# Optimization experiments

Measured on AMD Instinct MI355X. Metric: run time of the kernel, lower is better.

Reference implementation:

```python
import jax, jax.numpy as jnp
import numpy as np

D_MODEL, D_LOW, NUM_BINS = 512, 64, 39
DIST_MIN, DIST_MAX = 2.0, 22.0
BIN_WIDTH = (DIST_MAX - DIST_MIN) / (NUM_BINS - 1)
LN_EPS = 1e-5


def setup_inputs() -> dict:
    key = jax.random.key(0)
    ks = jax.random.split(key, 10)
    B, N = 2, 768
    h_res = jax.random.normal(ks[0], (B, N, D_MODEL), dtype=jnp.float32)
    # scale coords so pairwise distances span the [2, 22] bin range
    x_true = jax.random.normal(ks[1], (B, N, 3), dtype=jnp.float32) * 5.0
    token_pad_mask = jnp.ones((B, N), dtype=jnp.float32)
    s = 1.0 / np.sqrt(D_MODEL)
    return {
        "h_res": h_res,
        "x_true": x_true,
        "token_pad_mask": token_pad_mask,
        "ln_w": jnp.ones((D_MODEL,), jnp.float32),
        "ln_b": jnp.zeros((D_MODEL,), jnp.float32),
        "wu_w": jax.random.normal(ks[2], (D_LOW, D_MODEL), jnp.float32) * s,
        "wu_b": jnp.zeros((D_LOW,), jnp.float32),
        "wv_w": jax.random.normal(ks[3], (D_LOW, D_MODEL), jnp.float32) * s,
        "wv_b": jnp.zeros((D_LOW,), jnp.float32),
        "wb_w": jax.random.normal(ks[4], (NUM_BINS, D_LOW), jnp.float32) * (1.0 / np.sqrt(D_LOW)),
        "wb_b": jnp.zeros((NUM_BINS,), jnp.float32),
    }


def _layernorm(x, w, b):
    mu = jnp.mean(x, axis=-1, keepdims=True)
    var = jnp.mean(jnp.square(x - mu), axis=-1, keepdims=True)
    return (x - mu) * jax.lax.rsqrt(var + LN_EPS) * w + b


def reference(h_res, x_true, token_pad_mask, ln_w, ln_b, wu_w, wu_b, wv_w, wv_b, wb_w, wb_b):
    B, N, _ = h_res.shape
    # pairwise distances -> target bins (trunc-to-int then clamp, as torch .long())
    diff = x_true[:, :, None, :] - x_true[:, None, :, :]          # [B,N,N,3]
    d_true = jnp.sqrt(jnp.sum(diff * diff, axis=-1))               # [B,N,N]
    target = jnp.clip(((d_true - DIST_MIN) / BIN_WIDTH).astype(jnp.int32), 0, NUM_BINS - 1)

    h = _layernorm(h_res, ln_w, ln_b)
    U = h @ wu_w.T + wu_b                                          # [B,N,d_low]
    V = h @ wv_w.T + wv_b                                          # [B,N,d_low]
    # logits[b,i,j,k] = sum_c U[b,i,c] V[b,j,c] Wb[k,c] + bb[k]
    logits = jnp.einsum("bic,bjc,kc->bijk", U, V, wb_w) + wb_b     # [B,N,N,K]
    logp = jax.nn.log_softmax(logits, axis=-1)
    ce = -jnp.take_along_axis(logp, target[..., None], axis=-1)[..., 0]  # [B,N,N]

    mask = (token_pad_mask[:, :, None] * token_pad_mask[:, None, :]) > 0  # [B,N,N] bool
    counts = jnp.sum(mask, axis=(1, 2))                            # [B]
    per_sample = jnp.sum(jnp.where(mask, ce, 0.0), axis=(1, 2)) / jnp.maximum(counts, 1)
    valid = counts > 0
    total_count = jnp.sum(valid)
    loss = jnp.sum(jnp.where(valid, per_sample, 0.0)) / jnp.maximum(total_count, 1)
    return loss
```

## Files before the change

### kernel.cpp

```cpp
#include <hip/hip_runtime.h>
#include <hip/hip_bf16.h>
#include <math.h>

#define D_MODEL 512
#define D_LOW   64
#define NBINS   39
#define LOG2E   1.4426950408889634f
#define LN2     0.6931471805599453f

typedef __attribute__((ext_vector_type(8))) short short8;
typedef __attribute__((ext_vector_type(4))) float floatx4;

__global__ __launch_bounds__(256) void lnproj_tbin_kernel(
    const float* __restrict__ h_res,
    const float* __restrict__ ln_w, const float* __restrict__ ln_b,
    const float* __restrict__ wu_w, const float* __restrict__ wu_b,
    const float* __restrict__ wv_w, const float* __restrict__ wv_b,
    const float* __restrict__ x_true, const float* __restrict__ pmask,
    float* __restrict__ U, __hip_bfloat16* __restrict__ Vbf,
    signed char* __restrict__ tbg, int N, int B, int nLN, int TB) {
  const int tid = threadIdx.x;

  if ((int)blockIdx.x >= nLN) {
    const int idx   = blockIdx.x - nLN;
    const int NN    = N * N;
    const int total = B * NN;
    const float BW  = (22.0f - 2.0f) / 38.0f;
    for (int p = idx * 256 + tid; p < total; p += TB * 256) {
      const int b = p / NN;
      const int r = p - b * NN;
      const int i = r / N;
      const int j = r - i * N;
      const int rowi = b * N + i, rowj = b * N + j;
      const float dx = x_true[rowi * 3 + 0] - x_true[rowj * 3 + 0];
      const float dy = x_true[rowi * 3 + 1] - x_true[rowj * 3 + 1];
      const float dz = x_true[rowi * 3 + 2] - x_true[rowj * 3 + 2];
      const float d  = sqrtf(dx * dx + dy * dy + dz * dz);
      int tb = (int)((d - 2.0f) / BW);
      tb = tb < 0 ? 0 : (tb > NBINS - 1 ? NBINS - 1 : tb);
      const bool ok = (pmask[rowi] * pmask[rowj]) > 0.f;
      tbg[p] = ok ? (signed char)tb : (signed char)-1;
    }
    return;
  }

  const int wave = tid >> 6, lane = tid & 63;
  const int q = lane >> 4, ln16 = lane & 15;
  const int row0 = blockIdx.x * 16;
  const float* hp = h_res + (size_t)(row0 + ln16) * D_MODEL + q * 8;

  short8 abf[16];
  float sum = 0.f, ssq = 0.f;
  #pragma unroll
  for (int kc = 0; kc < 16; ++kc) {
    const floatx4 x0 = *reinterpret_cast<const floatx4*>(hp + kc * 32);
    const floatx4 x1 = *reinterpret_cast<const floatx4*>(hp + kc * 32 + 4);
    short8 a;
    #pragma unroll
    for (int e = 0; e < 4; ++e) {
      sum += x0[e]; ssq += x0[e] * x0[e];
      const __hip_bfloat16 hb = __float2bfloat16(x0[e]);
      a[e] = *reinterpret_cast<const short*>(&hb);
    }
    #pragma unroll
    for (int e = 0; e < 4; ++e) {
      sum += x1[e]; ssq += x1[e] * x1[e];
      const __hip_bfloat16 hb = __float2bfloat16(x1[e]);
      a[4 + e] = *reinterpret_cast<const short*>(&hb);
    }
    abf[kc] = a;
  }
  sum += __shfl_xor(sum, 16); sum += __shfl_xor(sum, 32);
  ssq += __shfl_xor(ssq, 16); ssq += __shfl_xor(ssq, 32);
  const float mu  = sum * (1.0f / (float)D_MODEL);
  const float var = ssq * (1.0f / (float)D_MODEL) - mu * mu;
  const float rs  = rsqrtf(var + 1e-5f);
  float mu_r[4], rs_r[4];
  #pragma unroll
  for (int r = 0; r < 4; ++r) {
    mu_r[r] = __shfl(mu, q * 4 + r);
    rs_r[r] = __shfl(rs, q * 4 + r);
  }

  const int obase = wave * 32;
  const int out0 = obase + ln16;
  const int out1 = obase + 16 + ln16;
  const float* wr0 = (out0 < 64) ? (wu_w + out0 * D_MODEL) : (wv_w + (out0 - 64) * D_MODEL);
  const float* wr1 = (out1 < 64) ? (wu_w + out1 * D_MODEL) : (wv_w + (out1 - 64) * D_MODEL);
  const float sc0 = (out0 < 64) ? LOG2E : 1.0f;
  const float sc1 = (out1 < 64) ? LOG2E : 1.0f;

  floatx4 acc0 = (floatx4){0.f, 0.f, 0.f, 0.f};
  floatx4 acc1 = (floatx4){0.f, 0.f, 0.f, 0.f};
  float s1a = 0.f, s1b = 0.f;
  float s2a = 0.f, s2b = 0.f;
  #pragma unroll
  for (int kc = 0; kc < 16; ++kc) {
    const int c0 = kc * 32 + q * 8;
    const floatx4 lw0 = *reinterpret_cast<const floatx4*>(ln_w + c0);
    const floatx4 lw1 = *reinterpret_cast<const floatx4*>(ln_w + c0 + 4);
    const floatx4 lb0 = *reinterpret_cast<const floatx4*>(ln_b + c0);
    const floatx4 lb1 = *reinterpret_cast<const floatx4*>(ln_b + c0 + 4);
    const floatx4 wa0 = *reinterpret_cast<const floatx4*>(wr0 + c0);
    const floatx4 wa1 = *reinterpret_cast<const floatx4*>(wr0 + c0 + 4);
    const floatx4 wb0 = *reinterpret_cast<const floatx4*>(wr1 + c0);
    const floatx4 wb1 = *reinterpret_cast<const floatx4*>(wr1 + c0 + 4);
    short8 b0, b1;
    #pragma unroll
    for (int e = 0; e < 4; ++e) {
      const float v0 = wa0[e] * lw0[e] * sc0;
      const float v1 = wa1[e] * lw1[e] * sc0;
      const __hip_bfloat16 h0 = __float2bfloat16(v0);
      const __hip_bfloat16 h1 = __float2bfloat16(v1);
      b0[e]     = *reinterpret_cast<const short*>(&h0);
      b0[4 + e] = *reinterpret_cast<const short*>(&h1);
      s1a += __bfloat162float(h0) + __bfloat162float(h1);
      s2a += wa0[e] * lb0[e] + wa1[e] * lb1[e];
      const float u0 = wb0[e] * lw0[e] * sc1;
      const float u1 = wb1[e] * lw1[e] * sc1;
      const __hip_bfloat16 g0 = __float2bfloat16(u0);
      const __hip_bfloat16 g1 = __float2bfloat16(u1);
      b1[e]     = *reinterpret_cast<const short*>(&g0);
      b1[4 + e] = *reinterpret_cast<const short*>(&g1);
      s1b += __bfloat162float(g0) + __bfloat162float(g1);
      s2b += wb0[e] * lb0[e] + wb1[e] * lb1[e];
    }
    acc0 = __builtin_amdgcn_mfma_f32_16x16x32_bf16(abf[kc], b0, acc0, 0, 0, 0);
    acc1 = __builtin_amdgcn_mfma_f32_16x16x32_bf16(abf[kc], b1, acc1, 0, 0, 0);
  }
  s1a += __shfl_xor(s1a, 16); s1a += __shfl_xor(s1a, 32);
  s1b += __shfl_xor(s1b, 16); s1b += __shfl_xor(s1b, 32);
  s2a += __shfl_xor(s2a, 16); s2a += __shfl_xor(s2a, 32);
  s2b += __shfl_xor(s2b, 16); s2b += __shfl_xor(s2b, 32);
  const float bias0 = sc0 * (((out0 < 64) ? wu_b[out0] : wv_b[out0 - 64]) + s2a);
  const float bias1 = sc1 * (((out1 < 64) ? wu_b[out1] : wv_b[out1 - 64]) + s2b);

  #pragma unroll
  for (int nt = 0; nt < 2; ++nt) {
    const int out  = nt ? out1 : out0;
    const floatx4 a = nt ? acc1 : acc0;
    const float ws = nt ? s1b : s1a;
    const float bb = nt ? bias1 : bias0;
    #pragma unroll
    for (int r = 0; r < 4; ++r) {
      const int rowg = row0 + q * 4 + r;
      const float val = rs_r[r] * a[r] - mu_r[r] * rs_r[r] * ws + bb;
      if (out < 64) {
        U[(size_t)rowg * D_LOW + out] = val;
      } else {
        Vbf[(size_t)rowg * D_LOW + (out - 64)] = __float2bfloat16(val);
      }
    }
  }
}

__global__ __launch_bounds__(256) void wprep_kernel(
    const float* __restrict__ U, const float* __restrict__ wb_w,
    short* __restrict__ wfragbuf, int BN) {
  __shared__ float wsh[NBINS * 65];
  const int tid = threadIdx.x;
  for (int e = tid; e < NBINS * D_LOW; e += 256) {
    const int n = e >> 6, c = e & 63;
    wsh[n * 65 + c] = wb_w[e];
  }
  __syncthreads();

  const int wave = tid >> 6, lane = tid & 63;
  const int q = lane >> 4, ln16 = lane & 15;
  const int rowi = blockIdx.x * 4 + wave;
  const float* Up = U + (size_t)rowi * D_LOW;

  float u[16];
  #pragma unroll
  for (int s = 0; s < 2; ++s)
    #pragma unroll
    for (int e = 0; e < 8; ++e) u[s * 8 + e] = Up[s * 32 + q * 8 + e];

  short* outp = wfragbuf + (size_t)rowi * 6 * 64 * 8;
  #pragma unroll
  for (int t = 0; t < 3; ++t) {
    const int n = t * 16 + ln16;
    #pragma unroll
    for (int s = 0; s < 2; ++s) {
      short8 f;
      #pragma unroll
      for (int e = 0; e < 8; ++e) {
        const float w = (n < NBINS) ? wsh[n * 65 + s * 32 + q * 8 + e] : 0.f;
        const float v = u[s * 8 + e] * w;
        const __hip_bfloat16 hb = __float2bfloat16(v);
        f[e] = *reinterpret_cast<const short*>(&hb);
      }
      *reinterpret_cast<short8*>(outp + ((size_t)(t * 2 + s) * 64 + lane) * 8) = f;
    }
  }
}

__global__ __launch_bounds__(256) void pair_mfma_kernel(
    const short* __restrict__ wfragbuf,
    const __hip_bfloat16* __restrict__ Vbf,
    const float* __restrict__ wb_b,
    const signed char* __restrict__ tbg,
    float* __restrict__ part, int N) {
  __shared__ float rbuf[8];
  const int i    = blockIdx.x;
  const int b    = blockIdx.y >> 1;
  const int half = blockIdx.y & 1;
  const int tid  = threadIdx.x;
  const int wave = tid >> 6, lane = tid & 63;
  const int q = lane >> 4, ln16 = lane & 15;
  const int rowi = b * N + i;

  short8 wfrag[3][2];
  {
    const short* wfp = wfragbuf + (size_t)rowi * 6 * 64 * 8;
    #pragma unroll
    for (int t = 0; t < 3; ++t)
      #pragma unroll
      for (int s = 0; s < 2; ++s)
        wfrag[t][s] = *reinterpret_cast<const short8*>(
            wfp + ((size_t)(t * 2 + s) * 64 + lane) * 8);
  }

  floatx4 bias_init[3];
  #pragma unroll
  for (int t = 0; t < 3; ++t)
    #pragma unroll
    for (int r = 0; r < 4; ++r) {
      const int bin = t * 16 + q * 4 + r;
      bias_init[t][r] = (bin < NBINS) ? LOG2E * wb_b[bin] : -INFINITY;
    }

  const short* Vp = reinterpret_cast<const short*>(Vbf) + (size_t)b * N * D_LOW;
  const signed char* tbp = tbg + (size_t)b * N * N + (size_t)i * N;
  const int jbase = half * 384 + wave * 96;
  const int q4 = q * 4;

  float ce_sum = 0.f, cnt_sum = 0.f;

  short8 v[2][2];
  int tbv[2];
  {
    #pragma unroll
    for (int tt = 0; tt < 2; ++tt) {
      const size_t jr = jbase + tt * 16 + ln16;
      v[tt][0] = *reinterpret_cast<const short8*>(Vp + jr * D_LOW + q * 8);
      v[tt][1] = *reinterpret_cast<const short8*>(Vp + jr * D_LOW + 32 + q * 8);
      tbv[tt]  = (int)tbp[jr];
    }
  }

  for (int g = 0; g < 3; ++g) {
    short8 vn[2][2];
    int tbn[2];
    if (g < 2) {
      const int jb = jbase + (g + 1) * 32;
      #pragma unroll
      for (int tt = 0; tt < 2; ++tt) {
        const size_t jr = jb + tt * 16 + ln16;
        vn[tt][0] = *reinterpret_cast<const short8*>(Vp + jr * D_LOW + q * 8);
        vn[tt][1] = *reinterpret_cast<const short8*>(Vp + jr * D_LOW + 32 + q * 8);
        tbn[tt]   = (int)tbp[jr];
      }
    }

    floatx4 f[2][3];
    #pragma unroll
    for (int tt = 0; tt < 2; ++tt)
      #pragma unroll
      for (int t = 0; t < 3; ++t) {
        floatx4 a = bias_init[t];
        a = __builtin_amdgcn_mfma_f32_16x16x32_bf16(wfrag[t][0], v[tt][0], a, 0, 0, 0);
        a = __builtin_amdgcn_mfma_f32_16x16x32_bf16(wfrag[t][1], v[tt][1], a, 0, 0, 0);
        f[tt][t] = a;
      }

    #pragma unroll
    for (int tt = 0; tt < 2; ++tt) {
      const int tb  = tbv[tt];
      const int tbq = tb - q4;
      float s0 = 0.f, s1 = 0.f, s2 = 0.f, s3 = 0.f, lt = 0.f;
      #pragma unroll
      for (int t = 0; t < 3; ++t) {
        const floatx4 fv = f[tt][t];
        s0 += __builtin_amdgcn_exp2f(fv[0]);
        s1 += __builtin_amdgcn_exp2f(fv[1]);
        s2 += __builtin_amdgcn_exp2f(fv[2]);
        s3 += __builtin_amdgcn_exp2f(fv[3]);
        lt += (tbq == t * 16 + 0) ? fv[0] : 0.f;
        lt += (tbq == t * 16 + 1) ? fv[1] : 0.f;
        lt += (tbq == t * 16 + 2) ? fv[2] : 0.f;
        lt += (tbq == t * 16 + 3) ? fv[3] : 0.f;
      }
      float ssum = (s0 + s1) + (s2 + s3);
      ssum += __shfl_xor(ssum, 16); ssum += __shfl_xor(ssum, 32);
      const float ok = (tb >= 0) ? 1.f : 0.f;
      ce_sum  += ok * LN2 * (__builtin_amdgcn_logf(ssum) - 4.0f * lt);
      cnt_sum += ok;
    }

    if (g < 2) {
      #pragma unroll
      for (int tt = 0; tt < 2; ++tt) {
        v[tt][0] = vn[tt][0]; v[tt][1] = vn[tt][1]; tbv[tt] = tbn[tt];
      }
    }
  }

  #pragma unroll
  for (int off = 32; off; off >>= 1) {
    ce_sum  += __shfl_xor(ce_sum, off);
    cnt_sum += __shfl_xor(cnt_sum, off);
  }
  if (lane == 0) { rbuf[wave] = ce_sum; rbuf[4 + wave] = cnt_sum; }
  __syncthreads();
  if (tid == 0) {
    const size_t slot = ((size_t)(b * 2 + half) * N + i) * 2;
    part[slot + 0] = rbuf[0] + rbuf[1] + rbuf[2] + rbuf[3];
    part[slot + 1] = rbuf[4] + rbuf[5] + rbuf[6] + rbuf[7];
  }
}

__global__ __launch_bounds__(256) void finalize_kernel(
    const float* __restrict__ part, float* __restrict__ out, int N, int B) {
  __shared__ float red[8];
  const int tid = threadIdx.x, wave = tid >> 6, lane = tid & 63;
  float loss = 0.f, vcount = 0.f;
  for (int b = 0; b < B; ++b) {
    float ce = 0.f, cnt = 0.f;
    for (int e = tid; e < 2 * N; e += 256) {
      const size_t base = ((size_t)b * 2 * N + e) * 2;
      ce  += part[base + 0];
      cnt += part[base + 1];
    }
    #pragma unroll
    for (int off = 32; off; off >>= 1) {
      ce  += __shfl_xor(ce, off);
      cnt += __shfl_xor(cnt, off);
    }
    if (lane == 0) { red[wave] = ce; red[4 + wave] = cnt; }
    __syncthreads();
    if (tid == 0) {
      const float s = red[0] + red[1] + red[2] + red[3];
      const float c = red[4] + red[5] + red[6] + red[7];
      if (c > 0.f) { loss += s / fmaxf(c, 1.f); vcount += 1.f; }
    }
    __syncthreads();
  }
  if (tid == 0) out[0] = (vcount > 0.f) ? loss / vcount : 0.f;
}

extern "C" void kernel_launch(void* const* d_in, const int* in_sizes, int n_in,
                              void* d_out, int out_size, void* d_ws, size_t ws_size,
                              hipStream_t stream) {
  const float* h_res  = (const float*)d_in[0];
  const float* x_true = (const float*)d_in[1];
  const float* pmask  = (const float*)d_in[2];
  const float* ln_w   = (const float*)d_in[3];
  const float* ln_b   = (const float*)d_in[4];
  const float* wu_w   = (const float*)d_in[5];
  const float* wu_b   = (const float*)d_in[6];
  const float* wv_w   = (const float*)d_in[7];
  const float* wv_b   = (const float*)d_in[8];
  const float* wb_w   = (const float*)d_in[9];
  const float* wb_b   = (const float*)d_in[10];

  const int B  = 2;
  const int N  = in_sizes[2] / B;
  const int BN = B * N;
  const int nLN = BN / 16;
  const int TB  = 160;

  float* U = (float*)d_ws;
  __hip_bfloat16* Vbf = (__hip_bfloat16*)(U + (size_t)BN * D_LOW);
  float* part = (float*)(Vbf + (size_t)BN * D_LOW);
  signed char* tbg = (signed char*)(part + 4 * (size_t)BN);
  short* wfragbuf = (short*)(tbg + (size_t)B * N * N);

  lnproj_tbin_kernel<<<nLN + TB, 256, 0, stream>>>(
      h_res, ln_w, ln_b, wu_w, wu_b, wv_w, wv_b, x_true, pmask,
      U, Vbf, tbg, N, B, nLN, TB);
  wprep_kernel<<<BN / 4, 256, 0, stream>>>(U, wb_w, wfragbuf, BN);
  pair_mfma_kernel<<<dim3(N, 2 * B), 256, 0, stream>>>(wfragbuf, Vbf, wb_b,
                                                       tbg, part, N);
  finalize_kernel<<<1, 256, 0, stream>>>(part, (float*)d_out, N, B);
}
```

Before: 125.6 us.

## Precompute LN-folded bf16 projection weights once and split LN-projection into its own kernel

Folding ln_w and the log2e scale into bf16 weights, plus the bias and weight-sum terms, moves into a new prep kernel that runs once per output column. Before, every row-tile block redid this work. The projection becomes a separate 64-thread kernel with four blocks per row tile, which loads the prepared bf16 fragments directly. Target-bin computation is restructured to one block per row i, so the per-element divisions and repeated x_i loads go away. The cost is one extra kernel launch and a dependency between prep and projection.

Result: faster. 118.5 us (-5.6%).

```diff
diff --git a/kernel.cpp b/kernel.cpp
--- a/kernel.cpp
+++ b/kernel.cpp
@@ -11,42 +11,79 @@
 typedef __attribute__((ext_vector_type(8))) short short8;
 typedef __attribute__((ext_vector_type(4))) float floatx4;
 
-__global__ __launch_bounds__(256) void lnproj_tbin_kernel(
-    const float* __restrict__ h_res,
+__global__ __launch_bounds__(256) void prep_tbin_kernel(
     const float* __restrict__ ln_w, const float* __restrict__ ln_b,
     const float* __restrict__ wu_w, const float* __restrict__ wu_b,
     const float* __restrict__ wv_w, const float* __restrict__ wv_b,
     const float* __restrict__ x_true, const float* __restrict__ pmask,
-    float* __restrict__ U, __hip_bfloat16* __restrict__ Vbf,
-    signed char* __restrict__ tbg, int N, int B, int nLN, int TB) {
+    __hip_bfloat16* __restrict__ w2bf, float* __restrict__ w2sum,
+    float* __restrict__ b2, signed char* __restrict__ tbg, int N) {
   const int tid = threadIdx.x;
 
-  if ((int)blockIdx.x >= nLN) {
-    const int idx   = blockIdx.x - nLN;
-    const int NN    = N * N;
-    const int total = B * NN;
+  if ((int)blockIdx.x >= 128) {
+    const int p = blockIdx.x - 128;
+    const int b = (p >= N) ? 1 : 0;
+    const int i = p - b * N;
+    const int rowi = b * N + i;
+    const float xi0 = x_true[rowi * 3 + 0];
+    const float xi1 = x_true[rowi * 3 + 1];
+    const float xi2 = x_true[rowi * 3 + 2];
+    const float pmi = pmask[rowi];
     const float BW  = (22.0f - 2.0f) / 38.0f;
-    for (int p = idx * 256 + tid; p < total; p += TB * 256) {
-      const int b = p / NN;
-      const int r = p - b * NN;
-      const int i = r / N;
-      const int j = r - i * N;
-      const int rowi = b * N + i, rowj = b * N + j;
-      const float dx = x_true[rowi * 3 + 0] - x_true[rowj * 3 + 0];
-      const float dy = x_true[rowi * 3 + 1] - x_true[rowj * 3 + 1];
-      const float dz = x_true[rowi * 3 + 2] - x_true[rowj * 3 + 2];
+    signed char* tbp = tbg + (size_t)b * N * N + (size_t)i * N;
+    for (int j = tid; j < N; j += 256) {
+      const int rowj = b * N + j;
+      const float dx = xi0 - x_true[rowj * 3 + 0];
+      const float dy = xi1 - x_true[rowj * 3 + 1];
+      const float dz = xi2 - x_true[rowj * 3 + 2];
       const float d  = sqrtf(dx * dx + dy * dy + dz * dz);
       int tb = (int)((d - 2.0f) / BW);
       tb = tb < 0 ? 0 : (tb > NBINS - 1 ? NBINS - 1 : tb);
-      const bool ok = (pmask[rowi] * pmask[rowj]) > 0.f;
-      tbg[p] = ok ? (signed char)tb : (signed char)-1;
+      tbp[j] = (pmi * pmask[rowj] > 0.f) ? (signed char)tb : (signed char)-1;
     }
     return;
   }
 
+  __shared__ float red[8];
+  const int o = blockIdx.x;
+  const bool isU = (o < 64);
+  const float* wrow = isU ? (wu_w + o * D_MODEL) : (wv_w + (o - 64) * D_MODEL);
+  const float scale = isU ? LOG2E : 1.0f;
+
+  float s1 = 0.f, s2 = 0.f;
+  #pragma unroll
+  for (int cc = 0; cc < 2; ++cc) {
+    const int c = tid + cc * 256;
+    const float w  = wrow[c];
+    const float w2 = w * ln_w[c] * scale;
+    const __hip_bfloat16 hb = __float2bfloat16(w2);
+    w2bf[o * D_MODEL + c] = hb;
+    s1 += __bfloat162float(hb);
+    s2 += w * ln_b[c];
+  }
+  #pragma unroll
+  for (int off = 32; off; off >>= 1) {
+    s1 += __shfl_xor(s1, off);
+    s2 += __shfl_xor(s2, off);
+  }
   const int wave = tid >> 6, lane = tid & 63;
+  if (lane == 0) { red[wave] = s1; red[4 + wave] = s2; }
+  __syncthreads();
+  if (tid == 0) {
+    w2sum[o] = red[0] + red[1] + red[2] + red[3];
+    const float ss2 = red[4] + red[5] + red[6] + red[7];
+    b2[o] = scale * ((isU ? wu_b[o] : wv_b[o - 64]) + ss2);
+  }
+}
+
+__global__ __launch_bounds__(64) void lnproj_kernel(
+    const float* __restrict__ h_res, const __hip_bfloat16* __restrict__ w2bf,
+    const float* __restrict__ w2sum, const float* __restrict__ b2,
+    float* __restrict__ U, __hip_bfloat16* __restrict__ Vbf, int N) {
+  const int lane = threadIdx.x;
   const int q = lane >> 4, ln16 = lane & 15;
-  const int row0 = blockIdx.x * 16;
+  const int rt = blockIdx.x >> 2, og = blockIdx.x & 3;
+  const int row0 = rt * 16;
   const float* hp = h_res + (size_t)(row0 + ln16) * D_MODEL + q * 8;
 
   short8 abf[16];
@@ -82,65 +119,28 @@
     rs_r[r] = __shfl(rs, q * 4 + r);
   }
 
-  const int obase = wave * 32;
+  const int obase = og * 32;
   const int out0 = obase + ln16;
   const int out1 = obase + 16 + ln16;
-  const float* wr0 = (out0 < 64) ? (wu_w + out0 * D_MODEL) : (wv_w + (out0 - 64) * D_MODEL);
-  const float* wr1 = (out1 < 64) ? (wu_w + out1 * D_MODEL) : (wv_w + (out1 - 64) * D_MODEL);
-  const float sc0 = (out0 < 64) ? LOG2E : 1.0f;
-  const float sc1 = (out1 < 64) ? LOG2E : 1.0f;
-
+  const short* wp = reinterpret_cast<const short*>(w2bf);
   floatx4 acc0 = (floatx4){0.f, 0.f, 0.f, 0.f};
   floatx4 acc1 = (floatx4){0.f, 0.f, 0.f, 0.f};
-  float s1a = 0.f, s1b = 0.f;
-  float s2a = 0.f, s2b = 0.f;
   #pragma unroll
   for (int kc = 0; kc < 16; ++kc) {
-    const int c0 = kc * 32 + q * 8;
-    const floatx4 lw0 = *reinterpret_cast<const floatx4*>(ln_w + c0);
-    const floatx4 lw1 = *reinterpret_cast<const floatx4*>(ln_w + c0 + 4);
-    const floatx4 lb0 = *reinterpret_cast<const floatx4*>(ln_b + c0);
-    const floatx4 lb1 = *reinterpret_cast<const floatx4*>(ln_b + c0 + 4);
-    const floatx4 wa0 = *reinterpret_cast<const floatx4*>(wr0 + c0);
-    const floatx4 wa1 = *reinterpret_cast<const floatx4*>(wr0 + c0 + 4);
-    const floatx4 wb0 = *reinterpret_cast<const floatx4*>(wr1 + c0);
-    const floatx4 wb1 = *reinterpret_cast<const floatx4*>(wr1 + c0 + 4);
-    short8 b0, b1;
-    #pragma unroll
-    for (int e = 0; e < 4; ++e) {
-      const float v0 = wa0[e] * lw0[e] * sc0;
-      const float v1 = wa1[e] * lw1[e] * sc0;
-      const __hip_bfloat16 h0 = __float2bfloat16(v0);
-      const __hip_bfloat16 h1 = __float2bfloat16(v1);
-      b0[e]     = *reinterpret_cast<const short*>(&h0);
-      b0[4 + e] = *reinterpret_cast<const short*>(&h1);
-      s1a += __bfloat162float(h0) + __bfloat162float(h1);
-      s2a += wa0[e] * lb0[e] + wa1[e] * lb1[e];
-      const float u0 = wb0[e] * lw0[e] * sc1;
-      const float u1 = wb1[e] * lw1[e] * sc1;
-      const __hip_bfloat16 g0 = __float2bfloat16(u0);
-      const __hip_bfloat16 g1 = __float2bfloat16(u1);
-      b1[e]     = *reinterpret_cast<const short*>(&g0);
-      b1[4 + e] = *reinterpret_cast<const short*>(&g1);
-      s1b += __bfloat162float(g0) + __bfloat162float(g1);
-      s2b += wb0[e] * lb0[e] + wb1[e] * lb1[e];
-    }
+    const short8 b0 = *reinterpret_cast<const short8*>(
+        wp + (size_t)out0 * D_MODEL + kc * 32 + q * 8);
+    const short8 b1 = *reinterpret_cast<const short8*>(
+        wp + (size_t)out1 * D_MODEL + kc * 32 + q * 8);
     acc0 = __builtin_amdgcn_mfma_f32_16x16x32_bf16(abf[kc], b0, acc0, 0, 0, 0);
     acc1 = __builtin_amdgcn_mfma_f32_16x16x32_bf16(abf[kc], b1, acc1, 0, 0, 0);
   }
-  s1a += __shfl_xor(s1a, 16); s1a += __shfl_xor(s1a, 32);
-  s1b += __shfl_xor(s1b, 16); s1b += __shfl_xor(s1b, 32);
-  s2a += __shfl_xor(s2a, 16); s2a += __shfl_xor(s2a, 32);
-  s2b += __shfl_xor(s2b, 16); s2b += __shfl_xor(s2b, 32);
-  const float bias0 = sc0 * (((out0 < 64) ? wu_b[out0] : wv_b[out0 - 64]) + s2a);
-  const float bias1 = sc1 * (((out1 < 64) ? wu_b[out1] : wv_b[out1 - 64]) + s2b);
 
   #pragma unroll
   for (int nt = 0; nt < 2; ++nt) {
     const int out  = nt ? out1 : out0;
     const floatx4 a = nt ? acc1 : acc0;
-    const float ws = nt ? s1b : s1a;
-    const float bb = nt ? bias1 : bias0;
+    const float ws = w2sum[out];
+    const float bb = b2[out];
     #pragma unroll
     for (int r = 0; r < 4; ++r) {
       const int rowg = row0 + q * 4 + r;
@@ -367,18 +367,21 @@
   const int B  = 2;
   const int N  = in_sizes[2] / B;
   const int BN = B * N;
-  const int nLN = BN / 16;
-  const int TB  = 160;
 
   float* U = (float*)d_ws;
   __hip_bfloat16* Vbf = (__hip_bfloat16*)(U + (size_t)BN * D_LOW);
   float* part = (float*)(Vbf + (size_t)BN * D_LOW);
   signed char* tbg = (signed char*)(part + 4 * (size_t)BN);
   short* wfragbuf = (short*)(tbg + (size_t)B * N * N);
-
-  lnproj_tbin_kernel<<<nLN + TB, 256, 0, stream>>>(
-      h_res, ln_w, ln_b, wu_w, wu_b, wv_w, wv_b, x_true, pmask,
-      U, Vbf, tbg, N, B, nLN, TB);
+  __hip_bfloat16* w2bf = (__hip_bfloat16*)(wfragbuf + (size_t)BN * 6 * 64 * 8);
+  float* w2sum = (float*)(w2bf + 128 * D_MODEL);
+  float* b2    = w2sum + 128;
+
+  prep_tbin_kernel<<<128 + BN, 256, 0, stream>>>(
+      ln_w, ln_b, wu_w, wu_b, wv_w, wv_b, x_true, pmask,
+      w2bf, w2sum, b2, tbg, N);
+  lnproj_kernel<<<(BN / 16) * 4, 64, 0, stream>>>(h_res, w2bf, w2sum, b2,
+                                                  U, Vbf, N);
   wprep_kernel<<<BN / 4, 256, 0, stream>>>(U, wb_w, wfragbuf, BN);
   pair_mfma_kernel<<<dim3(N, 2 * B), 256, 0, stream>>>(wfragbuf, Vbf, wb_b,
                                                        tbg, part, N);
```
